# Performance work log

Hardware: AMD Instinct MI355X
Metric: run time of the kernel (lower is better)

## Reference

```python
import jax, jax.numpy as jnp
import numpy as np

T, INPUT, OUTPUT, RES = 8192, 256, 256, 4096


def setup_inputs() -> dict:
    key = jax.random.key(0)
    k1, k2, k3, k4 = jax.random.split(key, 4)
    X = jax.random.normal(k1, (T, INPUT), dtype=jnp.float32)
    state0 = jnp.zeros((RES,), dtype=jnp.float32)
    # W_in ~ U(-1, 1), per the torch init
    W_in = jax.random.uniform(k2, (RES, INPUT), dtype=jnp.float32) * 2.0 - 1.0
    # Reservoir weights: signed uniform, scaled so spectral radius ~= 0.99.
    # A uniform(-1,1) R x R matrix has spectral radius ~ sqrt(R/3); divide it out.
    spectral_radius = 0.99
    W_res = (jax.random.uniform(k3, (RES, RES), dtype=jnp.float32) * 2.0 - 1.0)
    W_res = W_res * (spectral_radius / np.sqrt(RES / 3.0)).astype(np.float32)
    # Readout weights (normally fit by lstsq during training; random here)
    W_out = jax.random.normal(k4, (OUTPUT, RES), dtype=jnp.float32) * 0.02
    return {"X": X, "state0": state0, "W_in": W_in, "W_res": W_res, "W_out": W_out}


def reference(X, state0, W_in, W_res, W_out):
    # ESN inference loop: state_t = tanh(W_in @ x_t + W_res @ state_{t-1});
    # pred_t = W_out @ state_t. Strict sequential dependence -> lax.scan.
    def step(state, x):
        new_state = jnp.tanh(W_in @ x + W_res @ state)  # [RES]
        pred = W_out @ new_state                         # [OUTPUT]
        return new_state, pred

    _, preds = jax.lax.scan(step, state0, X)  # preds: [T, OUTPUT]
    return preds
```

## Files before the change

kernel.cpp:

```cpp
#include <hip/hip_runtime.h>

#define T_STEPS  8192
#define INPUT_N  256
#define OUTPUT_N 256
#define RES_N    4096
#define NB       256
#define NT       1024
#define RPB      16

#define PIN(x) asm volatile("" : "+v"(x))
#define PINU4(v) do { PIN((v).x); PIN((v).y); PIN((v).z); PIN((v).w); } while (0)

typedef unsigned long long ull;
typedef _Float16 half2v __attribute__((ext_vector_type(2)));

__device__ __forceinline__ unsigned pkf16(float lo, float hi) {
    return __builtin_bit_cast(unsigned, __builtin_amdgcn_cvt_pkrtz(lo, hi));
}
__device__ __forceinline__ float fdot2(unsigned w, unsigned s, float acc) {
    return __builtin_amdgcn_fdot2(__builtin_bit_cast(half2v, w),
                                  __builtin_bit_cast(half2v, s), acc, false);
}
__device__ __forceinline__ float fast_tanh(float x) {
    const float e = __expf(2.0f * x);
    return 1.0f - __fdividef(2.0f, e + 1.0f);
}

__global__ __launch_bounds__(NT)
void esn_persistent(
    const float* __restrict__ X,
    const float* __restrict__ state0,
    const float* __restrict__ W_in,
    const float* __restrict__ W_res,
    const float* __restrict__ W_out,
    float* __restrict__ out,
    unsigned* __restrict__ stbuf)
{
    const int tid  = threadIdx.x;
    const int bid  = blockIdx.x;
    const int wid  = tid >> 6;
    const int lane = tid & 63;
    const int qg   = lane >> 2;
    const int rg   = lane & 3;
    const int cg   = wid * 16 + qg;

    __shared__ unsigned w_lds[2 * 16 * 4 * 64 * 4];
    __shared__ float lds_part[2][16][20];
    __shared__ float lds_pp[2][16];

    float win[4];
#pragma unroll
    for (int r = 0; r < 4; ++r) {
        const int grow = bid * RPB + 4 * rg + r;
#pragma unroll
        for (int c = 0; c < 2; ++c) {
            const float* wr = W_res + (size_t)grow * RES_N + c * 2048 + 8 * cg;
            const float4 a = *(const float4*)wr;
            const float4 b = *(const float4*)(wr + 4);
            uint4 pk;
            pk.x = pkf16(a.x, a.y);
            pk.y = pkf16(a.z, a.w);
            pk.z = pkf16(b.x, b.y);
            pk.w = pkf16(b.z, b.w);
            ((uint4*)w_lds)[((c * 16 + wid) * 4 + r) * 64 + lane] = pk;
        }
        win[r] = W_in[(size_t)grow * INPUT_N + cg];
        PIN(win[r]);
    }
    unsigned wo[8];
#pragma unroll
    for (int m = 0; m < 8; ++m) {
        const int col = (m < 4) ? (8 * cg + 2 * m) : (2048 + 8 * cg + 2 * (m - 4));
        wo[m] = pkf16(W_out[(size_t)bid * RES_N + col],
                      W_out[(size_t)bid * RES_N + col + 1]);
        PIN(wo[m]);
    }

    const int ofs_base = ((rg < 2) ? (8 * cg) : (2048 + 8 * cg)) + 4 * (rg & 1);

    float xv = X[cg];

#pragma unroll 1
    for (int t = 0; t <= T_STEPS; ++t) {
        const int par  = t & 1;
        const int ppar = (t + 1) & 1;

        uint4 w[2][4];
#pragma unroll
        for (int c = 0; c < 2; ++c)
#pragma unroll
            for (int r = 0; r < 4; ++r) {
                w[c][r] = ((const uint4*)w_lds)[(((c * 16 + wid) * 4 + r) * 64) + lane];
                PINU4(w[c][r]);
            }

        unsigned d0, d1, d2, d3;
        if (t == 0) {
            const float4 q = *(const float4*)(state0 + ofs_base);
            d0 = pkf16(q.x, 0.f);
            d1 = pkf16(q.y, 0.f);
            d2 = pkf16(q.z, 0.f);
            d3 = pkf16(q.w, 0.f);
        } else {
            const unsigned exp = (unsigned)t;
            const ull* sp = (const ull*)(stbuf + (size_t)ppar * RES_N + ofs_base);
            for (;;) {
                const ull lo = __hip_atomic_load(sp, __ATOMIC_RELAXED,
                                                 __HIP_MEMORY_SCOPE_AGENT);
                const ull hi = __hip_atomic_load(sp + 1, __ATOMIC_RELAXED,
                                                 __HIP_MEMORY_SCOPE_AGENT);
                d0 = (unsigned)lo; d1 = (unsigned)(lo >> 32);
                d2 = (unsigned)hi; d3 = (unsigned)(hi >> 32);
                const unsigned tmin =
                    min(min(d0 >> 16, d1 >> 16), min(d2 >> 16, d3 >> 16));
                if (tmin >= exp) break;
                __builtin_amdgcn_s_sleep(1);
            }
        }

        const float xn = X[(size_t)((t + 1 < T_STEPS) ? (t + 1) : 0) * INPUT_N + cg];

        const unsigned pl0 = __builtin_amdgcn_perm(d1, d0, 0x05040100u);
        const unsigned pl1 = __builtin_amdgcn_perm(d3, d2, 0x05040100u);
        unsigned sp16[8];
#pragma unroll
        for (int m = 0; m < 8; ++m)
            sp16[m] = __shfl((m & 1) ? pl1 : pl0, (lane & 0x3C) | (m >> 1), 64);

        if (t < T_STEPS) {
            float p0 = win[0] * xv, p1 = win[1] * xv;
            float p2 = win[2] * xv, p3 = win[3] * xv;
#pragma unroll
            for (int c = 0; c < 2; ++c) {
                const unsigned s0 = sp16[4 * c + 0], s1 = sp16[4 * c + 1];
                const unsigned s2 = sp16[4 * c + 2], s3 = sp16[4 * c + 3];
                p0 = fdot2(w[c][0].x, s0, p0); p0 = fdot2(w[c][0].y, s1, p0);
                p0 = fdot2(w[c][0].z, s2, p0); p0 = fdot2(w[c][0].w, s3, p0);
                p1 = fdot2(w[c][1].x, s0, p1); p1 = fdot2(w[c][1].y, s1, p1);
                p1 = fdot2(w[c][1].z, s2, p1); p1 = fdot2(w[c][1].w, s3, p1);
                p2 = fdot2(w[c][2].x, s0, p2); p2 = fdot2(w[c][2].y, s1, p2);
                p2 = fdot2(w[c][2].z, s2, p2); p2 = fdot2(w[c][2].w, s3, p2);
                p3 = fdot2(w[c][3].x, s0, p3); p3 = fdot2(w[c][3].y, s1, p3);
                p3 = fdot2(w[c][3].z, s2, p3); p3 = fdot2(w[c][3].w, s3, p3);
            }
            p0 += __shfl_xor(p0, 4, 64); p1 += __shfl_xor(p1, 4, 64);
            p2 += __shfl_xor(p2, 4, 64); p3 += __shfl_xor(p3, 4, 64);
            p0 += __shfl_xor(p0, 8, 64); p1 += __shfl_xor(p1, 8, 64);
            p2 += __shfl_xor(p2, 8, 64); p3 += __shfl_xor(p3, 8, 64);
            float v = (qg & 1) ? ((qg & 2) ? p3 : p1)
                               : ((qg & 2) ? p2 : p0);
            v += __shfl_xor(v, 16, 64);
            v += __shfl_xor(v, 32, 64);
            if (lane < 16)
                lds_part[par][4 * (lane & 3) + (lane >> 2)][wid] = v;
        }
        __syncthreads();

        if (t < T_STEPS && wid == 15 && lane < 16) {
            const float4 a = *(const float4*)(&lds_part[par][lane][0]);
            const float4 b = *(const float4*)(&lds_part[par][lane][4]);
            const float4 c = *(const float4*)(&lds_part[par][lane][8]);
            const float4 d = *(const float4*)(&lds_part[par][lane][12]);
            const float s = ((a.x + a.y) + (a.z + a.w)) + ((b.x + b.y) + (b.z + b.w))
                          + ((c.x + c.y) + (c.z + c.w)) + ((d.x + d.y) + (d.z + d.w));
            const float ns = fast_tanh(s);
            const unsigned dw = pkf16(ns, 0.f) | ((unsigned)(t + 1) << 16);
            __hip_atomic_store(stbuf + (size_t)par * RES_N + bid * RPB + lane,
                               dw, __ATOMIC_RELAXED, __HIP_MEMORY_SCOPE_AGENT);
        }

        if (t >= 2 && wid == 14 && lane < 16) {
            float pv = lds_pp[ppar][lane];
            pv += __shfl_xor(pv, 8, 64);
            pv += __shfl_xor(pv, 4, 64);
            pv += __shfl_xor(pv, 2, 64);
            pv += __shfl_xor(pv, 1, 64);
            if (lane == 0) out[(size_t)(t - 2) * OUTPUT_N + bid] = pv;
        }

        if (t > 0) {
            float pp = 0.f;
            if (rg == 0) {
#pragma unroll
                for (int m = 0; m < 8; ++m) pp = fdot2(wo[m], sp16[m], pp);
            }
            pp += __shfl_xor(pp, 4, 64);
            pp += __shfl_xor(pp, 8, 64);
            pp += __shfl_xor(pp, 16, 64);
            pp += __shfl_xor(pp, 32, 64);
            if (lane == 0) lds_pp[par][wid] = pp;
        }

        xv = xn;
    }

    __syncthreads();
    if (wid == 14 && lane < 16) {
        float pv = lds_pp[T_STEPS & 1][lane];
        pv += __shfl_xor(pv, 8, 64);
        pv += __shfl_xor(pv, 4, 64);
        pv += __shfl_xor(pv, 2, 64);
        pv += __shfl_xor(pv, 1, 64);
        if (lane == 0) out[(size_t)(T_STEPS - 1) * OUTPUT_N + bid] = pv;
    }
}

extern "C" void kernel_launch(void* const* d_in, const int* in_sizes, int n_in,
                              void* d_out, int out_size, void* d_ws, size_t ws_size,
                              hipStream_t stream) {
    const float* X      = (const float*)d_in[0];
    const float* state0 = (const float*)d_in[1];
    const float* W_in   = (const float*)d_in[2];
    const float* W_res  = (const float*)d_in[3];
    const float* W_out  = (const float*)d_in[4];
    float* out = (float*)d_out;

    unsigned* stbuf = (unsigned*)d_ws;

    (void)hipMemsetAsync(stbuf, 0, 2 * RES_N * sizeof(unsigned), stream);

    esn_persistent<<<dim3(NB), dim3(NT), 0, stream>>>(
        X, state0, W_in, W_res, W_out, out, stbuf);
}
```

Before: 17.58 ms.

## Replace per-step block barrier with LDS atomic accumulation and last-arriver publish

Removes the per-timestep __syncthreads. Each wave now atomically adds its partial row sums into LDS and bumps a per-parity counter, and the last wave to arrive applies tanh and publishes the new state to global memory. Without the block-wide barrier, fast waves no longer wait for slow ones and the critical path to publishing state may shorten. In exchange, float atomic adds make the summation order nondeterministic, and correctness depends on LDS ordering assumptions and the lds_pp read being hoisted before the barrier's removal.

```diff
diff --git a/kernel.cpp b/kernel.cpp
--- a/kernel.cpp
+++ b/kernel.cpp
@@ -45,8 +45,12 @@
     const int cg   = wid * 16 + qg;
 
     __shared__ unsigned w_lds[2 * 16 * 4 * 64 * 4];
-    __shared__ float lds_part[2][16][20];
-    __shared__ float lds_pp[2][16];
+    __shared__ float    lds_acc[2][16];
+    __shared__ float    lds_pp[2][16];
+    __shared__ unsigned lds_cnt[2];
+
+    if (tid < 2) lds_cnt[tid] = 0u;
+    if (tid < 32) lds_acc[tid >> 4][tid & 15] = 0.f;
 
     float win[4];
 #pragma unroll
@@ -75,6 +79,7 @@
                       W_out[(size_t)bid * RES_N + col + 1]);
         PIN(wo[m]);
     }
+    __syncthreads();
 
     const int ofs_base = ((rg < 2) ? (8 * cg) : (2048 + 8 * cg)) + 4 * (rg & 1);
 
@@ -120,6 +125,10 @@
 
         const float xn = X[(size_t)((t + 1 < T_STEPS) ? (t + 1) : 0) * INPUT_N + cg];
 
+        float pv = 0.f;
+        const bool do_out = (t >= 2 && wid == 14);
+        if (do_out && lane < 16) pv = lds_pp[ppar][lane];
+
         const unsigned pl0 = __builtin_amdgcn_perm(d1, d0, 0x05040100u);
         const unsigned pl1 = __builtin_amdgcn_perm(d3, d2, 0x05040100u);
         unsigned sp16[8];
@@ -152,43 +161,45 @@
             v += __shfl_xor(v, 16, 64);
             v += __shfl_xor(v, 32, 64);
             if (lane < 16)
-                lds_part[par][4 * (lane & 3) + (lane >> 2)][wid] = v;
-        }
-        __syncthreads();
-
-        if (t < T_STEPS && wid == 15 && lane < 16) {
-            const float4 a = *(const float4*)(&lds_part[par][lane][0]);
-            const float4 b = *(const float4*)(&lds_part[par][lane][4]);
-            const float4 c = *(const float4*)(&lds_part[par][lane][8]);
-            const float4 d = *(const float4*)(&lds_part[par][lane][12]);
-            const float s = ((a.x + a.y) + (a.z + a.w)) + ((b.x + b.y) + (b.z + b.w))
-                          + ((c.x + c.y) + (c.z + c.w)) + ((d.x + d.y) + (d.z + d.w));
-            const float ns = fast_tanh(s);
-            const unsigned dw = pkf16(ns, 0.f) | ((unsigned)(t + 1) << 16);
-            __hip_atomic_store(stbuf + (size_t)par * RES_N + bid * RPB + lane,
-                               dw, __ATOMIC_RELAXED, __HIP_MEMORY_SCOPE_AGENT);
-        }
-
-        if (t >= 2 && wid == 14 && lane < 16) {
-            float pv = lds_pp[ppar][lane];
+                unsafeAtomicAdd(&lds_acc[par][4 * (lane & 3) + (lane >> 2)], v);
+        }
+
+        if (t > 0) {
+            float pp = 0.f;
+            if (rg == 0) {
+#pragma unroll
+                for (int m = 0; m < 8; ++m) pp = fdot2(wo[m], sp16[m], pp);
+            }
+            pp += __shfl_xor(pp, 4, 64);
+            pp += __shfl_xor(pp, 8, 64);
+            pp += __shfl_xor(pp, 16, 64);
+            pp += __shfl_xor(pp, 32, 64);
+            if (lane == 0) lds_pp[par][wid] = pp;
+        }
+
+        if (t < T_STEPS) {
+            asm volatile("s_waitcnt lgkmcnt(0)" ::: "memory");
+            unsigned old = 0;
+            if (lane == 0) old = atomicAdd(&lds_cnt[par], 1u);
+            old = __shfl(old, 0, 64);
+            if (old == 16u * (unsigned)(t >> 1) + 15u) {
+                if (lane < 16) {
+                    const float s = lds_acc[par][lane];
+                    const float ns = fast_tanh(s);
+                    const unsigned dw = pkf16(ns, 0.f) | ((unsigned)(t + 1) << 16);
+                    __hip_atomic_store(stbuf + (size_t)par * RES_N + bid * RPB + lane,
+                                       dw, __ATOMIC_RELAXED, __HIP_MEMORY_SCOPE_AGENT);
+                    lds_acc[par][lane] = 0.f;
+                }
+            }
+        }
+
+        if (do_out) {
             pv += __shfl_xor(pv, 8, 64);
             pv += __shfl_xor(pv, 4, 64);
             pv += __shfl_xor(pv, 2, 64);
             pv += __shfl_xor(pv, 1, 64);
             if (lane == 0) out[(size_t)(t - 2) * OUTPUT_N + bid] = pv;
-        }
-
-        if (t > 0) {
-            float pp = 0.f;
-            if (rg == 0) {
-#pragma unroll
-                for (int m = 0; m < 8; ++m) pp = fdot2(wo[m], sp16[m], pp);
-            }
-            pp += __shfl_xor(pp, 4, 64);
-            pp += __shfl_xor(pp, 8, 64);
-            pp += __shfl_xor(pp, 16, 64);
-            pp += __shfl_xor(pp, 32, 64);
-            if (lane == 0) lds_pp[par][wid] = pp;
         }
 
         xv = xn;
```

Result: slower. 31.55 ms (+79.5%).
